# Kernel optimization log

Measured on AMD Instinct MI355X. Metric: run time of the kernel, lower is better.

## Reference

```python
import jax, jax.numpy as jnp
import numpy as np

B, S, H, NH = 2, 2048, 1024, 16
HD = H // NH  # head_size = 64


def setup_inputs() -> dict:
    key = jax.random.key(0)
    ks = jax.random.split(key, 9)
    sc = 0.02
    return {
        "hidden_states": jax.random.normal(ks[0], (B, S, H), dtype=jnp.float32),
        "Wq": jax.random.normal(ks[1], (H, H), dtype=jnp.float32) * sc,
        "bq": jax.random.normal(ks[2], (H,), dtype=jnp.float32) * sc,
        "Wk": jax.random.normal(ks[3], (H, H), dtype=jnp.float32) * sc,
        "bk": jax.random.normal(ks[4], (H,), dtype=jnp.float32) * sc,
        "Wv": jax.random.normal(ks[5], (H, H), dtype=jnp.float32) * sc,
        "bv": jax.random.normal(ks[6], (H,), dtype=jnp.float32) * sc,
        "Wo": jax.random.normal(ks[7], (H, H), dtype=jnp.float32) * sc,
        "bo": jax.random.normal(ks[8], (H,), dtype=jnp.float32) * sc,
    }


def reference(hidden_states, Wq, bq, Wk, bk, Wv, bv, Wo, bo):
    b, s, h = hidden_states.shape
    # nn.Linear: y = x @ W.T + b
    q = hidden_states @ Wq.T + bq
    k = hidden_states @ Wk.T + bk
    v = hidden_states @ Wv.T + bv
    q = q.reshape(b, s, NH, HD)
    k = k.reshape(b, s, NH, HD)
    v = v.reshape(b, s, NH, HD)
    # scores: [b, heads, q, k]
    scores = jnp.einsum("bqhd,bkhd->bhqk", q, k) / jnp.sqrt(jnp.float32(HD))
    # causal mask: triu(ones, diagonal=1) positions set to -inf
    causal = jnp.triu(jnp.ones((s, s), dtype=bool), k=1)
    scores = jnp.where(causal[None, None], -jnp.inf, scores)
    attn = jax.nn.softmax(scores, axis=-1)
    ctx = jnp.einsum("bhqk,bkhd->bqhd", attn, v).reshape(b, s, h)
    return ctx @ Wo.T + bo
```

## Files before the change

kernel.cpp:

```cpp
#include <hip/hip_runtime.h>
#include <hip/hip_bf16.h>

#define B_  2
#define S_  2048
#define H_  1024
#define NH_ 16
#define HD_ 64

typedef unsigned short u16;
typedef unsigned int   u32;
typedef __attribute__((ext_vector_type(4)))  float  f32x4;
typedef __attribute__((ext_vector_type(16))) float  f32x16;
typedef __attribute__((ext_vector_type(8)))  __bf16 bf16x8;
typedef __attribute__((ext_vector_type(4)))  unsigned int u32x4;
typedef __attribute__((ext_vector_type(4)))  unsigned short u16x4;

__device__ __forceinline__ u16 f2bf(float f) {
  unsigned u = __builtin_bit_cast(unsigned, f);
  u += 0x7fffu + ((u >> 16) & 1u);
  return (u16)(u >> 16);
}
__device__ __forceinline__ u32 cvtpk(float lo, float hi) {
  u32 r;
  asm("v_cvt_pk_bf16_f32 %0, %1, %2" : "=v"(r) : "v"(lo), "v"(hi));
  return r;
}
__device__ __forceinline__ float ex2(float x) {
  float r;
  asm("v_exp_f32 %0, %1" : "=v"(r) : "v"(x));
  return r;
}

__device__ __forceinline__ void gload_lds16(const void* g, void* l) {
  __builtin_amdgcn_global_load_lds(
      (const __attribute__((address_space(1))) void*)g,
      (__attribute__((address_space(3))) void*)l, 16, 0, 0);
}

#define NX_ (4u * 1024u * 1024u)
__global__ __launch_bounds__(256) void cvt_all(const float* __restrict__ x,
                                               const float* __restrict__ w0, const float* __restrict__ w1,
                                               const float* __restrict__ w2, const float* __restrict__ w3,
                                               u16* __restrict__ xb,
                                               u16* __restrict__ o0, u16* __restrict__ o1,
                                               u16* __restrict__ o2, u16* __restrict__ o3) {
  size_t i4 = ((size_t)blockIdx.x * 256 + threadIdx.x) * 4;
  const float* src; u16* dst; size_t off;
  if (i4 < (size_t)NX_) { src = x; dst = xb; off = i4; }
  else {
    size_t j = i4 - NX_;
    int seg = (int)(j >> 20);
    off = j & ((1u << 20) - 1);
    src = seg == 0 ? w0 : seg == 1 ? w1 : seg == 2 ? w2 : w3;
    dst = seg == 0 ? o0 : seg == 1 ? o1 : seg == 2 ? o2 : o3;
  }
  float4 v = *reinterpret_cast<const float4*>(src + off);
  u16x4 o;
  o[0] = f2bf(v.x); o[1] = f2bf(v.y); o[2] = f2bf(v.z); o[3] = f2bf(v.w);
  *reinterpret_cast<u16x4*>(dst + off) = o;
}

__device__ __forceinline__ void store_out(float* C, size_t idx, float v) { C[idx] = v; }
__device__ __forceinline__ void store_out(u16* C, size_t idx, float v) { C[idx] = f2bf(v); }

template <int MI, typename OutT>
__device__ __forceinline__ void gemm_core(const u16* __restrict__ A, const u16* __restrict__ Bw,
                                          const float* __restrict__ bias, OutT* __restrict__ C,
                                          int M, int N, int K, float oscale, int m0, int n0,
                                          u16* lsA, u16* lsB) {
  const int t = threadIdx.x;
  const int w = t >> 6, lane = t & 63;
  const int g = lane >> 4, c = lane & 15;
  const int wr = w >> 1, wc = w & 1;

  f32x4 acc[MI][4] = {};
  const int rowS = w * 16 + (lane >> 2);
  const int sgr  = (lane & 3) ^ ((lane >> 2) & 3) ^ ((lane >> 4) & 3);
  const int colS = sgr * 8;
  const int rcol = (g ^ (c & 3) ^ ((c >> 2) & 3)) * 8;

  for (int k0 = 0; k0 < K; k0 += 32) {
    __syncthreads();
#pragma unroll
    for (int r = 0; r < MI / 2; ++r)
      gload_lds16(A + (size_t)(m0 + r * 64 + rowS) * K + k0 + colS, lsA + r * 2048 + w * 512);
#pragma unroll
    for (int r = 0; r < 2; ++r)
      gload_lds16(Bw + (size_t)(n0 + r * 64 + rowS) * K + k0 + colS, lsB + r * 2048 + w * 512);
    asm volatile("s_waitcnt vmcnt(0)" ::: "memory");
    __syncthreads();

    bf16x8 af[MI], bfr[4];
#pragma unroll
    for (int mi = 0; mi < MI; ++mi)
      af[mi] = *reinterpret_cast<const bf16x8*>(&lsA[(wr * (MI * 16) + mi * 16 + c) * 32 + rcol]);
#pragma unroll
    for (int ni = 0; ni < 4; ++ni)
      bfr[ni] = *reinterpret_cast<const bf16x8*>(&lsB[(wc * 64 + ni * 16 + c) * 32 + rcol]);
#pragma unroll
    for (int mi = 0; mi < MI; ++mi)
#pragma unroll
      for (int ni = 0; ni < 4; ++ni)
        acc[mi][ni] = __builtin_amdgcn_mfma_f32_16x16x32_bf16(af[mi], bfr[ni], acc[mi][ni], 0, 0, 0);
  }

#pragma unroll
  for (int mi = 0; mi < MI; ++mi) {
    int rowb = m0 + wr * (MI * 16) + mi * 16 + g * 4;
#pragma unroll
    for (int ni = 0; ni < 4; ++ni) {
      int col = n0 + wc * 64 + ni * 16 + c;
      float bv = bias[col];
#pragma unroll
      for (int r = 0; r < 4; ++r) {
        float v = (acc[mi][ni][r] + bv) * oscale;
        store_out(C, (size_t)(rowb + r) * N + col, v);
      }
    }
  }
}

__global__ __launch_bounds__(256) void gemm_qkv(const u16* __restrict__ xb,
                                                const u16* __restrict__ Wq, const u16* __restrict__ Wk,
                                                const u16* __restrict__ Wv,
                                                const float* __restrict__ bq, const float* __restrict__ bk,
                                                const float* __restrict__ bv,
                                                u16* __restrict__ Q, u16* __restrict__ Kb, u16* __restrict__ Vb,
                                                int M, int K, float qscale) {
  __shared__ u16 lsA[4096];
  __shared__ u16 lsB[4096];
  const int fid = blockIdx.x;
  const int xcd = fid & 7, i = fid >> 3;
  const int mloc = i / 24, nn = i % 24;
  const int m0 = (xcd * 4 + mloc) * 128;
  const int ng = nn * 128;
  const int sel = ng >> 10, n0 = ng & 1023;
  const u16*  W    = sel == 0 ? Wq : sel == 1 ? Wk : Wv;
  const float* bia = sel == 0 ? bq : sel == 1 ? bk : bv;
  u16*        Cp   = sel == 0 ? Q  : sel == 1 ? Kb : Vb;
  float os = sel == 0 ? qscale : 1.0f;
  gemm_core<4, u16>(xb, W, bia, Cp, M, 1024, K, os, m0, n0, lsA, lsB);
}

__global__ __launch_bounds__(256) void gemm_wo(const u16* __restrict__ A, const u16* __restrict__ Bw,
                                               const float* __restrict__ bias, float* __restrict__ C,
                                               int M, int N, int K) {
  __shared__ u16 lsA[2048];
  __shared__ u16 lsB[4096];
  const int fid = blockIdx.x;
  const int xcd = fid & 7, i = fid >> 3;
  const int mloc = i >> 3, nn = i & 7;
  const int m0 = (xcd * 8 + mloc) * 64;
  const int n0 = nn * 128;
  gemm_core<2, float>(A, Bw, bias, C, M, N, K, 1.0f, m0, n0, lsA, lsB);
}

__global__ __launch_bounds__(256, 4) void attn_fwd(const u16* __restrict__ Qg,
                                                   const u16* __restrict__ Kg,
                                                   const u16* __restrict__ Vg,
                                                   u16* __restrict__ Og) {
  __shared__ __align__(16) u16 smem[18432];
  u16* lsKb = smem;
  u16* lsVb = smem + 8192;
  float* lsO  = (float*)smem;
  float* lsML = (float*)((char*)smem + 20480);
  u16*   lsOT = smem + 10752;

  const int blk = blockIdx.x;
  const int xcd = blk & 7, i = blk >> 3;
  const int pj = i & 15, bgrp = i >> 4;
  const int bh = xcd * 4 + bgrp;
  const int h = bh & 15, b = bh >> 4;

  const int t = threadIdx.x, w = t >> 6, lane = t & 63;
  const int c5 = lane & 31, hi = lane >> 5;
  const int sub = w & 1, par = w >> 1;
  const size_t headoff = (size_t)b * (S_ * H_) + (size_t)h * HD_;

  const int sp = w & 1, sh = w >> 1;
  const int kRowLoc = 16 * sh + (lane >> 3);
  const int kSrcCol = ((lane & 7) ^ (lane >> 3)) << 4;
  const int vKvLoc  = 16 * sh + 2 * (lane >> 3);
  const int vD0     = 8 * (lane & 7);
  const int vKvx    = vKvLoc ^ (((lane & 7) & 3) << 3);

  int qkOff[4];
#pragma unroll
  for (int kc = 0; kc < 4; ++kc)
    qkOff[kc] = c5 * 128 + ((32 * kc + 16 * hi) ^ ((c5 & 7) << 4));
  const int pvRow0 = c5 * 80, pvRow1 = (32 + c5) * 80;
  int pvCol[2];
#pragma unroll
  for (int kp2 = 0; kp2 < 2; ++kp2)
    pvCol[kp2] = 2 * ((16 * kp2 + 8 * hi) ^ ((c5 >> 3) << 3));

  u32x4 vA, vB;
  auto STAGE = [&](int m) {
    const int kv0 = m * 64 + 32 * sp;
    const u16* vp = Vg + headoff + (size_t)(kv0 + vKvLoc) * H_ + vD0;
    vA = *reinterpret_cast<const u32x4*>(vp);
    vB = *reinterpret_cast<const u32x4*>(vp + H_);
    char* kt = (char*)(lsKb + ((m & 1) * 2 + sp) * 2048) + 16 * sh * 128;
    const char* ks = (const char*)(Kg + headoff + (size_t)(kv0 + kRowLoc) * H_) + kSrcCol;
    gload_lds16(ks, kt);
    gload_lds16(ks + 8 * (H_ * 2), kt + 8 * 128);
  };
  auto WRITEVT = [&](int m) {
    u16* vt = lsVb + ((m & 1) * 2 + sp) * 2560;
#pragma unroll
    for (int jj = 0; jj < 4; ++jj) {
      u32 lo  = __builtin_amdgcn_perm(vB[jj], vA[jj], 0x05040100u);
      u32 hi2 = __builtin_amdgcn_perm(vB[jj], vA[jj], 0x07060302u);
      *reinterpret_cast<u32*>(vt + (vD0 + 2 * jj) * 40 + vKvx)     = lo;
      *reinterpret_cast<u32*>(vt + (vD0 + 2 * jj + 1) * 40 + vKvx) = hi2;
    }
  };

  for (int seg = 0; seg < 2; ++seg) {
    const int qt = seg ? pj : 31 - pj;
    const int q0w = qt * 64 + 32 * sub;
    if (seg) __syncthreads();

    bf16x8 aq[4];
#pragma unroll
    for (int kc = 0; kc < 4; ++kc)
      aq[kc] = *reinterpret_cast<const bf16x8*>(Qg + headoff + (size_t)(q0w + c5) * H_ + kc * 16 + hi * 8);

    f32x16 o0 = {}, o1 = {};
    float mrun = -1e30f, lrun = 0.f;

    STAGE(0);
    asm volatile("s_waitcnt vmcnt(2)" ::: "memory");
    WRITEVT(0);
    asm volatile("s_waitcnt lgkmcnt(0)" ::: "memory");
    asm volatile("s_waitcnt vmcnt(0)" ::: "memory");
    __builtin_amdgcn_s_barrier();

    for (int n = 0; n <= qt; ++n) {
      const int buf = n & 1;
      const bool st = n < qt;
      if (st) STAGE(n + 1);

      const bool live = (2 * n + par) <= (2 * qt + sub);
      const bool diag = (2 * n + par) == (2 * qt + sub);
      f32x16 sc = {};
      if (live) {
        const char* kb = (const char*)(lsKb + (buf * 2 + par) * 2048);
        __builtin_amdgcn_s_setprio(1);
#pragma unroll
        for (int kc = 0; kc < 4; ++kc) {
          bf16x8 ak = *reinterpret_cast<const bf16x8*>(kb + qkOff[kc]);
          sc = __builtin_amdgcn_mfma_f32_32x32x16_bf16(ak, aq[kc], sc, 0, 0, 0);
        }
        __builtin_amdgcn_s_setprio(0);
        if (diag) {
#pragma unroll
          for (int r = 0; r < 16; ++r) {
            int kvl = (r & 3) + 8 * (r >> 2) + 4 * hi;
            sc[r] = (kvl > c5) ? -1e30f : sc[r];
          }
        }
        float pm = sc[0];
#pragma unroll
        for (int r = 1; r < 16; ++r) pm = fmaxf(pm, sc[r]);
        pm = fmaxf(pm, (float)__shfl_xor(pm, 32));
        if (!__all(pm <= mrun + 8.0f)) {
          float mn = fmaxf(mrun, pm);
          float s8 = ex2(mrun - mn);
          mrun = mn; lrun *= s8;
#pragma unroll
          for (int r = 0; r < 16; ++r) { o0[r] *= s8; o1[r] *= s8; }
        }
      }

      if (st) {
        asm volatile("s_waitcnt vmcnt(2)" ::: "memory");
        WRITEVT(n + 1);
      }

      if (live) {
        const char* vtb = (const char*)(lsVb + (buf * 2 + par) * 2560);
        float rs = 0.f;
        u32 wd0[2], wd1[2], wd2[2], wd3[2];
#pragma unroll
        for (int a = 0; a < 4; ++a) {
          float p0 = ex2(sc[4 * a + 0] - mrun), p1 = ex2(sc[4 * a + 1] - mrun);
          float p2 = ex2(sc[4 * a + 2] - mrun), p3 = ex2(sc[4 * a + 3] - mrun);
          rs += (p0 + p1) + (p2 + p3);
          u32* wdp = a == 0 ? wd0 : a == 1 ? wd1 : a == 2 ? wd2 : wd3;
          wdp[0] = cvtpk(p0, p1);
          wdp[1] = cvtpk(p2, p3);
        }
        rs += (float)__shfl_xor(rs, 32);
        lrun += rs;
        __builtin_amdgcn_s_setprio(1);
#pragma unroll
        for (int kp2 = 0; kp2 < 2; ++kp2) {
          u32 wa0 = kp2 ? wd2[0] : wd0[0], wa1 = kp2 ? wd2[1] : wd0[1];
          u32 wb0 = kp2 ? wd3[0] : wd1[0], wb1 = kp2 ? wd3[1] : wd1[1];
          u32 own0 = hi ? wb0 : wa0, own1 = hi ? wb1 : wa1;
          u32 snd0 = hi ? wa0 : wb0, snd1 = hi ? wa1 : wb1;
          u32 oth0 = (u32)__shfl_xor((int)snd0, 32);
          u32 oth1 = (u32)__shfl_xor((int)snd1, 32);
          u32x4 pw;
          pw[0] = hi ? oth0 : own0;
          pw[1] = hi ? oth1 : own1;
          pw[2] = hi ? own0 : oth0;
          pw[3] = hi ? own1 : oth1;
          bf16x8 pb = __builtin_bit_cast(bf16x8, pw);
          bf16x8 av0 = *reinterpret_cast<const bf16x8*>(vtb + pvRow0 + pvCol[kp2]);
          bf16x8 av1 = *reinterpret_cast<const bf16x8*>(vtb + pvRow1 + pvCol[kp2]);
          o0 = __builtin_amdgcn_mfma_f32_32x32x16_bf16(av0, pb, o0, 0, 0, 0);
          o1 = __builtin_amdgcn_mfma_f32_32x32x16_bf16(av1, pb, o1, 0, 0, 0);
        }
        __builtin_amdgcn_s_setprio(0);
      }

      asm volatile("s_waitcnt lgkmcnt(0)" ::: "memory");
      if (st) asm volatile("s_waitcnt vmcnt(0)" ::: "memory");
      __builtin_amdgcn_s_barrier();
    }

    if (par == 0) {
      if (hi == 0) { lsML[sub * 64 + c5] = mrun; lsML[sub * 64 + 32 + c5] = lrun; }
#pragma unroll
      for (int dt = 0; dt < 2; ++dt) {
        float* dst = lsO + ((size_t)((sub * 2 + dt) * 64 + lane)) * 20;
        const f32x16& oo = dt ? o1 : o0;
#pragma unroll
        for (int k4 = 0; k4 < 4; ++k4) {
          f32x4 v4 = {oo[4 * k4], oo[4 * k4 + 1], oo[4 * k4 + 2], oo[4 * k4 + 3]};
          *reinterpret_cast<f32x4*>(dst + 4 * k4) = v4;
        }
      }
    }
    __syncthreads();
    if (par == 1) {
      float mA = lsML[sub * 64 + c5];
      float lA = lsML[sub * 64 + 32 + c5];
      float mn = fmaxf(mA, mrun);
      float sA = ex2(mA - mn), sB = ex2(mrun - mn);
      float linv = 1.0f / (lA * sA + lrun * sB);
      sA *= linv; sB *= linv;
      u16* ot = lsOT + sub * 2304;
#pragma unroll
      for (int dt = 0; dt < 2; ++dt) {
        const float* sp2 = lsO + ((size_t)((sub * 2 + dt) * 64 + lane)) * 20;
        f32x4 a4[4];
#pragma unroll
        for (int k4 = 0; k4 < 4; ++k4) a4[k4] = *reinterpret_cast<const f32x4*>(sp2 + 4 * k4);
        const f32x16& oo = dt ? o1 : o0;
#pragma unroll
        for (int a = 0; a < 4; ++a)
#pragma unroll
          for (int u = 0; u < 2; ++u) {
            int r = 4 * a + 2 * u;
            float e0 = a4[a][2 * u]     * sA + oo[r]     * sB;
            float e1 = a4[a][2 * u + 1] * sA + oo[r + 1] * sB;
            int d = 32 * dt + 8 * a + 4 * hi + 2 * u;
            *reinterpret_cast<u32*>(ot + c5 * 72 + d) = cvtpk(e0, e1);
          }
      }
      asm volatile("s_waitcnt lgkmcnt(0)" ::: "memory");
      __builtin_amdgcn_sched_barrier(0);
#pragma unroll
      for (int rr = 0; rr < 4; ++rr) {
        int q = 8 * rr + (lane >> 3);
        int d8 = (lane & 7) * 8;
        u32x4 vv = *reinterpret_cast<const u32x4*>(ot + q * 72 + d8);
        *reinterpret_cast<u32x4*>(Og + headoff + (size_t)(qt * 64 + 32 * sub + q) * H_ + d8) = vv;
      }
    }
  }
}

extern "C" void kernel_launch(void* const* d_in, const int* in_sizes, int n_in,
                              void* d_out, int out_size, void* d_ws, size_t ws_size,
                              hipStream_t stream) {
  const float* x  = (const float*)d_in[0];
  const float* Wq = (const float*)d_in[1];
  const float* bq = (const float*)d_in[2];
  const float* Wk = (const float*)d_in[3];
  const float* bk = (const float*)d_in[4];
  const float* Wv = (const float*)d_in[5];
  const float* bv = (const float*)d_in[6];
  const float* Wo = (const float*)d_in[7];
  const float* bo = (const float*)d_in[8];
  float* out = (float*)d_out;

  const size_t MT = (size_t)B_ * S_;
  char* p = (char*)d_ws;
  u16* xb  = (u16*)p; p += MT * H_ * 2;
  u16* Wqb = (u16*)p; p += (size_t)H_ * H_ * 2;
  u16* Wkb = (u16*)p; p += (size_t)H_ * H_ * 2;
  u16* Wvb = (u16*)p; p += (size_t)H_ * H_ * 2;
  u16* Wob = (u16*)p; p += (size_t)H_ * H_ * 2;
  u16* Qb  = (u16*)p; p += MT * H_ * 2;
  u16* Kb  = (u16*)p; p += MT * H_ * 2;
  u16* Vb  = (u16*)p; p += MT * H_ * 2;
  u16* Cb  = xb;

  cvt_all<<<8192, 256, 0, stream>>>(x, Wq, Wk, Wv, Wo, xb, Wqb, Wkb, Wvb, Wob);

  const float qscale = 0.125f * 1.44269504088896f;
  gemm_qkv<<<768, 256, 0, stream>>>(xb, Wqb, Wkb, Wvb, bq, bk, bv,
                                    Qb, Kb, Vb, (int)MT, H_, qscale);

  attn_fwd<<<512, 256, 0, stream>>>(Qb, Kb, Vb, Cb);

  gemm_wo<<<512, 256, 0, stream>>>(Cb, Wob, bo, out, (int)MT, H_, H_);
}
```

Measured before the change: 112.7 us.

## Split attention KV range across two blocks with a separate merge kernel

Templates the attention kernel so each query tile's KV loop is split into interleaved halves handled by separate blocks. This doubles the grid from 512 to 1024 blocks to raise occupancy and balance load. Each half writes unnormalized fp32 partial outputs plus max and sum statistics to workspace, and a new merge kernel combines them into bf16. The cost is an extra kernel launch and the fp32 partial-output traffic. The split path is used only when the workspace is large enough, otherwise the original single-pass path runs.

```diff
diff --git a/kernel.cpp b/kernel.cpp
--- a/kernel.cpp
+++ b/kernel.cpp
@@ -9,6 +9,7 @@
 
 typedef unsigned short u16;
 typedef unsigned int   u32;
+typedef __attribute__((ext_vector_type(2)))  float  f32x2;
 typedef __attribute__((ext_vector_type(4)))  float  f32x4;
 typedef __attribute__((ext_vector_type(16))) float  f32x16;
 typedef __attribute__((ext_vector_type(8)))  __bf16 bf16x8;
@@ -155,10 +156,13 @@
   gemm_core<2, float>(A, Bw, bias, C, M, N, K, 1.0f, m0, n0, lsA, lsB);
 }
 
+template <int HALVES>
 __global__ __launch_bounds__(256, 4) void attn_fwd(const u16* __restrict__ Qg,
                                                    const u16* __restrict__ Kg,
                                                    const u16* __restrict__ Vg,
-                                                   u16* __restrict__ Og) {
+                                                   u16* __restrict__ Og,
+                                                   float* __restrict__ Op,
+                                                   float* __restrict__ Ml) {
   __shared__ __align__(16) u16 smem[18432];
   u16* lsKb = smem;
   u16* lsVb = smem + 8192;
@@ -168,7 +172,9 @@
 
   const int blk = blockIdx.x;
   const int xcd = blk & 7, i = blk >> 3;
-  const int pj = i & 15, bgrp = i >> 4;
+  int pj, bgrp, half;
+  if (HALVES == 2) { half = i & 1; pj = (i >> 1) & 15; bgrp = (i >> 5) & 3; }
+  else             { half = 0;     pj = i & 15;        bgrp = i >> 4;       }
   const int bh = xcd * 4 + bgrp;
   const int h = bh & 15, b = bh >> 4;
 
@@ -195,18 +201,18 @@
     pvCol[kp2] = 2 * ((16 * kp2 + 8 * hi) ^ ((c5 >> 3) << 3));
 
   u32x4 vA, vB;
-  auto STAGE = [&](int m) {
+  auto STAGE = [&](int m, int buf) {
     const int kv0 = m * 64 + 32 * sp;
     const u16* vp = Vg + headoff + (size_t)(kv0 + vKvLoc) * H_ + vD0;
     vA = *reinterpret_cast<const u32x4*>(vp);
     vB = *reinterpret_cast<const u32x4*>(vp + H_);
-    char* kt = (char*)(lsKb + ((m & 1) * 2 + sp) * 2048) + 16 * sh * 128;
+    char* kt = (char*)(lsKb + (buf * 2 + sp) * 2048) + 16 * sh * 128;
     const char* ks = (const char*)(Kg + headoff + (size_t)(kv0 + kRowLoc) * H_) + kSrcCol;
     gload_lds16(ks, kt);
     gload_lds16(ks + 8 * (H_ * 2), kt + 8 * 128);
   };
-  auto WRITEVT = [&](int m) {
-    u16* vt = lsVb + ((m & 1) * 2 + sp) * 2560;
+  auto WRITEVT = [&](int buf) {
+    u16* vt = lsVb + (buf * 2 + sp) * 2560;
 #pragma unroll
     for (int jj = 0; jj < 4; ++jj) {
       u32 lo  = __builtin_amdgcn_perm(vB[jj], vA[jj], 0x05040100u);
@@ -229,17 +235,18 @@
     f32x16 o0 = {}, o1 = {};
     float mrun = -1e30f, lrun = 0.f;
 
-    STAGE(0);
+    STAGE(half, 0);
     asm volatile("s_waitcnt vmcnt(2)" ::: "memory");
     WRITEVT(0);
     asm volatile("s_waitcnt lgkmcnt(0)" ::: "memory");
     asm volatile("s_waitcnt vmcnt(0)" ::: "memory");
     __builtin_amdgcn_s_barrier();
 
-    for (int n = 0; n <= qt; ++n) {
-      const int buf = n & 1;
-      const bool st = n < qt;
-      if (st) STAGE(n + 1);
+    int it = 0;
+    for (int n = half; n <= qt; n += HALVES, ++it) {
+      const int buf = it & 1;
+      const bool st = (n + HALVES) <= qt;
+      if (st) STAGE(n + HALVES, buf ^ 1);
 
       const bool live = (2 * n + par) <= (2 * qt + sub);
       const bool diag = (2 * n + par) == (2 * qt + sub);
@@ -275,7 +282,7 @@
 
       if (st) {
         asm volatile("s_waitcnt vmcnt(2)" ::: "memory");
-        WRITEVT(n + 1);
+        WRITEVT(buf ^ 1);
       }
 
       if (live) {
@@ -340,37 +347,96 @@
       float lA = lsML[sub * 64 + 32 + c5];
       float mn = fmaxf(mA, mrun);
       float sA = ex2(mA - mn), sB = ex2(mrun - mn);
-      float linv = 1.0f / (lA * sA + lrun * sB);
-      sA *= linv; sB *= linv;
-      u16* ot = lsOT + sub * 2304;
-#pragma unroll
-      for (int dt = 0; dt < 2; ++dt) {
-        const float* sp2 = lsO + ((size_t)((sub * 2 + dt) * 64 + lane)) * 20;
-        f32x4 a4[4];
-#pragma unroll
-        for (int k4 = 0; k4 < 4; ++k4) a4[k4] = *reinterpret_cast<const f32x4*>(sp2 + 4 * k4);
-        const f32x16& oo = dt ? o1 : o0;
-#pragma unroll
-        for (int a = 0; a < 4; ++a)
-#pragma unroll
-          for (int u = 0; u < 2; ++u) {
-            int r = 4 * a + 2 * u;
-            float e0 = a4[a][2 * u]     * sA + oo[r]     * sB;
-            float e1 = a4[a][2 * u + 1] * sA + oo[r + 1] * sB;
-            int d = 32 * dt + 8 * a + 4 * hi + 2 * u;
-            *reinterpret_cast<u32*>(ot + c5 * 72 + d) = cvtpk(e0, e1);
-          }
-      }
-      asm volatile("s_waitcnt lgkmcnt(0)" ::: "memory");
-      __builtin_amdgcn_sched_barrier(0);
-#pragma unroll
-      for (int rr = 0; rr < 4; ++rr) {
-        int q = 8 * rr + (lane >> 3);
-        int d8 = (lane & 7) * 8;
-        u32x4 vv = *reinterpret_cast<const u32x4*>(ot + q * 72 + d8);
-        *reinterpret_cast<u32x4*>(Og + headoff + (size_t)(qt * 64 + 32 * sub + q) * H_ + d8) = vv;
+      float lcomb = lA * sA + lrun * sB;
+
+      if constexpr (HALVES == 1) {
+        float linv = 1.0f / lcomb;
+        float sAn = sA * linv, sBn = sB * linv;
+        u16* ot = lsOT + sub * 2304;
+#pragma unroll
+        for (int dt = 0; dt < 2; ++dt) {
+          const float* sp2 = lsO + ((size_t)((sub * 2 + dt) * 64 + lane)) * 20;
+          f32x4 a4[4];
+#pragma unroll
+          for (int k4 = 0; k4 < 4; ++k4) a4[k4] = *reinterpret_cast<const f32x4*>(sp2 + 4 * k4);
+          const f32x16& oo = dt ? o1 : o0;
+#pragma unroll
+          for (int a = 0; a < 4; ++a)
+#pragma unroll
+            for (int u = 0; u < 2; ++u) {
+              int r = 4 * a + 2 * u;
+              float e0 = a4[a][2 * u]     * sAn + oo[r]     * sBn;
+              float e1 = a4[a][2 * u + 1] * sAn + oo[r + 1] * sBn;
+              int d = 32 * dt + 8 * a + 4 * hi + 2 * u;
+              *reinterpret_cast<u32*>(ot + c5 * 72 + d) = cvtpk(e0, e1);
+            }
+        }
+        asm volatile("s_waitcnt lgkmcnt(0)" ::: "memory");
+        __builtin_amdgcn_sched_barrier(0);
+#pragma unroll
+        for (int rr = 0; rr < 4; ++rr) {
+          int q = 8 * rr + (lane >> 3);
+          int d8 = (lane & 7) * 8;
+          u32x4 vv = *reinterpret_cast<const u32x4*>(lsOT + sub * 2304 + q * 72 + d8);
+          *reinterpret_cast<u32x4*>(Og + headoff + (size_t)(qt * 64 + 32 * sub + q) * H_ + d8) = vv;
+        }
+      } else {
+        const size_t pidx = (size_t)((bh * 32 + qt) * 2 + half);
+        float* Opb = Op + pidx * 4096;
+        float* Mlb = Ml + pidx * 128;
+        const int ql = 32 * sub + c5;
+        if (hi == 0) { Mlb[ql] = mn; Mlb[64 + ql] = lcomb; }
+#pragma unroll
+        for (int dt = 0; dt < 2; ++dt) {
+          const float* sp2 = lsO + ((size_t)((sub * 2 + dt) * 64 + lane)) * 20;
+          f32x4 a4[4];
+#pragma unroll
+          for (int k4 = 0; k4 < 4; ++k4) a4[k4] = *reinterpret_cast<const f32x4*>(sp2 + 4 * k4);
+          const f32x16& oo = dt ? o1 : o0;
+#pragma unroll
+          for (int a = 0; a < 4; ++a)
+#pragma unroll
+            for (int u = 0; u < 2; ++u) {
+              int r = 4 * a + 2 * u;
+              f32x2 e;
+              e[0] = a4[a][2 * u]     * sA + oo[r]     * sB;
+              e[1] = a4[a][2 * u + 1] * sA + oo[r + 1] * sB;
+              int d = 32 * dt + 8 * a + 4 * hi + 2 * u;
+              *reinterpret_cast<f32x2*>(Opb + ql * 64 + d) = e;
+            }
+        }
       }
     }
+  }
+}
+
+__global__ __launch_bounds__(256) void attn_merge(const float* __restrict__ Op,
+                                                  const float* __restrict__ Ml,
+                                                  u16* __restrict__ Og) {
+  const int idx = blockIdx.x;
+  const int bh = idx >> 5, qt = idx & 31;
+  const int h = bh & 15, b = bh >> 4;
+  const int t = threadIdx.x;
+  const int q = t >> 2, d0 = (t & 3) * 16;
+  const float* ml0 = Ml + (size_t)(idx * 2 + 0) * 128;
+  const float* ml1 = Ml + (size_t)(idx * 2 + 1) * 128;
+  float m0 = ml0[q], l0 = ml0[64 + q];
+  float m1 = ml1[q], l1 = ml1[64 + q];
+  float mn = fmaxf(m0, m1);
+  float s0 = ex2(m0 - mn), s1 = ex2(m1 - mn);
+  float inv = 1.0f / (l0 * s0 + l1 * s1);
+  s0 *= inv; s1 *= inv;
+  const float* p0 = Op + (size_t)(idx * 2 + 0) * 4096 + q * 64 + d0;
+  const float* p1 = Op + (size_t)(idx * 2 + 1) * 4096 + q * 64 + d0;
+  u16* og = Og + (size_t)b * (S_ * H_) + (size_t)(qt * 64 + q) * H_ + (size_t)h * HD_ + d0;
+#pragma unroll
+  for (int k = 0; k < 4; ++k) {
+    f32x4 a = *reinterpret_cast<const f32x4*>(p0 + 4 * k);
+    f32x4 c = *reinterpret_cast<const f32x4*>(p1 + 4 * k);
+    u16x4 o;
+#pragma unroll
+    for (int j = 0; j < 4; ++j) o[j] = f2bf(a[j] * s0 + c[j] * s1);
+    *reinterpret_cast<u16x4*>(og + 4 * k) = o;
   }
 }
 
@@ -398,7 +464,12 @@
   u16* Qb  = (u16*)p; p += MT * H_ * 2;
   u16* Kb  = (u16*)p; p += MT * H_ * 2;
   u16* Vb  = (u16*)p; p += MT * H_ * 2;
+  float* Opart = (float*)p; p += (size_t)2048 * 4096 * 4;
+  float* Mlpart = (float*)p; p += (size_t)2048 * 128 * 4;
   u16* Cb  = xb;
+
+  const size_t need = (size_t)(p - (char*)d_ws);
+  const bool split = ws_size >= need;
 
   cvt_all<<<8192, 256, 0, stream>>>(x, Wq, Wk, Wv, Wo, xb, Wqb, Wkb, Wvb, Wob);
 
@@ -406,7 +477,12 @@
   gemm_qkv<<<768, 256, 0, stream>>>(xb, Wqb, Wkb, Wvb, bq, bk, bv,
                                     Qb, Kb, Vb, (int)MT, H_, qscale);
 
-  attn_fwd<<<512, 256, 0, stream>>>(Qb, Kb, Vb, Cb);
+  if (split) {
+    attn_fwd<2><<<1024, 256, 0, stream>>>(Qb, Kb, Vb, Cb, Opart, Mlpart);
+    attn_merge<<<1024, 256, 0, stream>>>(Opart, Mlpart, Cb);
+  } else {
+    attn_fwd<1><<<512, 256, 0, stream>>>(Qb, Kb, Vb, Cb, Opart, Mlpart);
+  }
 
   gemm_wo<<<512, 256, 0, stream>>>(Cb, Wob, bo, out, (int)MT, H_, H_);
 }
```

After: 115.4 us (median of 3 runs). 2.4% more time.

## Deepen attention K/V prefetch to a three-stage LDS ring buffer

Applied to the files above, without the earlier changes.

Moves the attention kernel's K/V staging from double buffering to a three-buffer rotation, so tile n+2 is prefetched while n+1 is transposed into LDS and n is computed. The loop is unrolled by two to alternate register sets holding the in-flight V data, and the vmcnt waits are relaxed to keep more loads outstanding. LDS per block grows, and launch bounds drop from 4 to 2 blocks per SM, which lowers occupancy in exchange for more latency hiding.

```diff
diff --git a/kernel.cpp b/kernel.cpp
--- a/kernel.cpp
+++ b/kernel.cpp
@@ -155,13 +155,13 @@
   gemm_core<2, float>(A, Bw, bias, C, M, N, K, 1.0f, m0, n0, lsA, lsB);
 }
 
-__global__ __launch_bounds__(256, 4) void attn_fwd(const u16* __restrict__ Qg,
+__global__ __launch_bounds__(256, 2) void attn_fwd(const u16* __restrict__ Qg,
                                                    const u16* __restrict__ Kg,
                                                    const u16* __restrict__ Vg,
                                                    u16* __restrict__ Og) {
-  __shared__ __align__(16) u16 smem[18432];
+  __shared__ __align__(16) u16 smem[27648];
   u16* lsKb = smem;
-  u16* lsVb = smem + 8192;
+  u16* lsVb = smem + 12288;
   float* lsO  = (float*)smem;
   float* lsML = (float*)((char*)smem + 20480);
   u16*   lsOT = smem + 10752;
@@ -194,23 +194,22 @@
   for (int kp2 = 0; kp2 < 2; ++kp2)
     pvCol[kp2] = 2 * ((16 * kp2 + 8 * hi) ^ ((c5 >> 3) << 3));
 
-  u32x4 vA, vB;
-  auto STAGE = [&](int m) {
+  auto STAGE = [&](int m, int kbuf, u32x4& A, u32x4& B) {
     const int kv0 = m * 64 + 32 * sp;
     const u16* vp = Vg + headoff + (size_t)(kv0 + vKvLoc) * H_ + vD0;
-    vA = *reinterpret_cast<const u32x4*>(vp);
-    vB = *reinterpret_cast<const u32x4*>(vp + H_);
-    char* kt = (char*)(lsKb + ((m & 1) * 2 + sp) * 2048) + 16 * sh * 128;
+    A = *reinterpret_cast<const u32x4*>(vp);
+    B = *reinterpret_cast<const u32x4*>(vp + H_);
+    char* kt = (char*)(lsKb + (kbuf * 2 + sp) * 2048) + 16 * sh * 128;
     const char* ks = (const char*)(Kg + headoff + (size_t)(kv0 + kRowLoc) * H_) + kSrcCol;
     gload_lds16(ks, kt);
     gload_lds16(ks + 8 * (H_ * 2), kt + 8 * 128);
   };
-  auto WRITEVT = [&](int m) {
-    u16* vt = lsVb + ((m & 1) * 2 + sp) * 2560;
+  auto WRITEVT = [&](int vbuf, const u32x4& A, const u32x4& B) {
+    u16* vt = lsVb + (vbuf * 2 + sp) * 2560;
 #pragma unroll
     for (int jj = 0; jj < 4; ++jj) {
-      u32 lo  = __builtin_amdgcn_perm(vB[jj], vA[jj], 0x05040100u);
-      u32 hi2 = __builtin_amdgcn_perm(vB[jj], vA[jj], 0x07060302u);
+      u32 lo  = __builtin_amdgcn_perm(B[jj], A[jj], 0x05040100u);
+      u32 hi2 = __builtin_amdgcn_perm(B[jj], A[jj], 0x07060302u);
       *reinterpret_cast<u32*>(vt + (vD0 + 2 * jj) * 40 + vKvx)     = lo;
       *reinterpret_cast<u32*>(vt + (vD0 + 2 * jj + 1) * 40 + vKvx) = hi2;
     }
@@ -228,24 +227,26 @@
 
     f32x16 o0 = {}, o1 = {};
     float mrun = -1e30f, lrun = 0.f;
-
-    STAGE(0);
-    asm volatile("s_waitcnt vmcnt(2)" ::: "memory");
-    WRITEVT(0);
+    u32x4 vA0, vB0, vA1, vB1;
+    int bufs0 = 0, bufs1 = 1, bufs2 = 2;
+
+    STAGE(0, 0, vA0, vB0);
+    asm volatile("s_waitcnt vmcnt(0)" ::: "memory");
+    WRITEVT(0, vA0, vB0);
+    if (qt >= 1) STAGE(1, 1, vA1, vB1);
     asm volatile("s_waitcnt lgkmcnt(0)" ::: "memory");
-    asm volatile("s_waitcnt vmcnt(0)" ::: "memory");
     __builtin_amdgcn_s_barrier();
 
-    for (int n = 0; n <= qt; ++n) {
-      const int buf = n & 1;
-      const bool st = n < qt;
-      if (st) STAGE(n + 1);
+    auto body = [&](int n, u32x4& sA, u32x4& sB, u32x4& wAr, u32x4& wBr) {
+      const bool st1 = (n + 1 <= qt);
+      const bool st2 = (n + 2 <= qt);
+      if (st2) STAGE(n + 2, bufs2, sA, sB);
 
       const bool live = (2 * n + par) <= (2 * qt + sub);
       const bool diag = (2 * n + par) == (2 * qt + sub);
       f32x16 sc = {};
       if (live) {
-        const char* kb = (const char*)(lsKb + (buf * 2 + par) * 2048);
+        const char* kb = (const char*)(lsKb + (bufs0 * 2 + par) * 2048);
         __builtin_amdgcn_s_setprio(1);
 #pragma unroll
         for (int kc = 0; kc < 4; ++kc) {
@@ -273,13 +274,12 @@
         }
       }
 
-      if (st) {
-        asm volatile("s_waitcnt vmcnt(2)" ::: "memory");
-        WRITEVT(n + 1);
-      }
+      if (st2)      asm volatile("s_waitcnt vmcnt(4)" ::: "memory");
+      else if (st1) asm volatile("s_waitcnt vmcnt(0)" ::: "memory");
+      if (st1) WRITEVT(bufs1, wAr, wBr);
 
       if (live) {
-        const char* vtb = (const char*)(lsVb + (buf * 2 + par) * 2560);
+        const char* vtb = (const char*)(lsVb + (bufs0 * 2 + par) * 2560);
         float rs = 0.f;
         u32 wd0[2], wd1[2], wd2[2], wd3[2];
 #pragma unroll
@@ -317,8 +317,13 @@
       }
 
       asm volatile("s_waitcnt lgkmcnt(0)" ::: "memory");
-      if (st) asm volatile("s_waitcnt vmcnt(0)" ::: "memory");
       __builtin_amdgcn_s_barrier();
+      int tmp = bufs0; bufs0 = bufs1; bufs1 = bufs2; bufs2 = tmp;
+    };
+
+    for (int n = 0; n <= qt; n += 2) {
+      body(n, vA0, vB0, vA1, vB1);
+      if (n + 1 <= qt) body(n + 1, vA1, vB1, vA0, vB0);
     }
 
     if (par == 0) {
@@ -367,7 +372,7 @@
       for (int rr = 0; rr < 4; ++rr) {
         int q = 8 * rr + (lane >> 3);
         int d8 = (lane & 7) * 8;
-        u32x4 vv = *reinterpret_cast<const u32x4*>(ot + q * 72 + d8);
+        u32x4 vv = *reinterpret_cast<const u32x4*>(lsOT + sub * 2304 + q * 72 + d8);
         *reinterpret_cast<u32x4*>(Og + headoff + (size_t)(qt * 64 + 32 * sub + q) * H_ + d8) = vv;
       }
     }
```

New measurement: 115.0 us. +2.1%, slower.
